# Optimization experiments

Hardware: AMD Instinct MI355X
Metric: run time of the kernel (lower is better)

Reference implementation:

```python
import jax, jax.numpy as jnp
import numpy as np

HEAD_SIZE = 64
N_EMBD = 768

def setup_inputs() -> dict:
    key = jax.random.key(0)
    k1, k2, k3, k4 = jax.random.split(key, 4)
    x = jax.random.normal(k1, (8, 2048, N_EMBD), dtype=jnp.float32)
    # nn.Linear weights are [out, in]; we store transposed [in, out] for x @ W
    scale = 1.0 / np.sqrt(N_EMBD)
    Wk = jax.random.uniform(k2, (N_EMBD, HEAD_SIZE), jnp.float32, -scale, scale)
    Wq = jax.random.uniform(k3, (N_EMBD, HEAD_SIZE), jnp.float32, -scale, scale)
    Wv = jax.random.uniform(k4, (N_EMBD, HEAD_SIZE), jnp.float32, -scale, scale)
    return {"x": x, "Wk": Wk, "Wq": Wq, "Wv": Wv}

def reference(x, Wk, Wq, Wv):
    # x: [B, T, C]
    k = x @ Wk  # [B, T, H]
    q = x @ Wq  # [B, T, H]
    v = x @ Wv  # [B, T, H]
    inv_sqrt_h = jnp.asarray(k.shape[-1], x.dtype) ** -0.5
    att = jnp.einsum('bth,bsh->bts', q, k) * inv_sqrt_h  # [B, T, T]
    att = jax.nn.softmax(att, axis=-1)  # no causal mask in original
    out = jnp.einsum('bts,bsh->bth', att, v)  # [B, T, H]
    return out
```

## Files before the change

### kernel.cpp

```cpp
#include <hip/hip_runtime.h>
#include <hip/hip_bf16.h>


#define SEQ   2048
#define CEMB  768
#define SCL 0.18033688011112042f
#define THR 11.0f

typedef __attribute__((ext_vector_type(4))) float f32x4;
typedef __attribute__((ext_vector_type(4))) float fvec4;
typedef __attribute__((ext_vector_type(8))) short short8;
typedef __attribute__((ext_vector_type(4))) short short4v;
typedef __attribute__((ext_vector_type(4))) unsigned short u16x4;
typedef __attribute__((ext_vector_type(2))) unsigned int u32x2;
typedef __attribute__((ext_vector_type(4))) unsigned int u32x4;

#define MFMA32 __builtin_amdgcn_mfma_f32_16x16x32_bf16

__device__ __forceinline__ unsigned short f2bf(float f) {
    unsigned int u = __builtin_bit_cast(unsigned int, f);
    u += 0x7fffu + ((u >> 16) & 1u);
    return (unsigned short)(u >> 16);
}
__device__ __forceinline__ unsigned int pack_bf2(float lo, float hi) {
    unsigned int ulo = __builtin_bit_cast(unsigned int, lo);
    unsigned int uhi = __builtin_bit_cast(unsigned int, hi);
    return ((uhi + 0x8000u) & 0xffff0000u) | ((ulo + 0x8000u) >> 16);
}
__device__ __forceinline__ short8 pack8(fvec4 a, fvec4 b) {
    short8 s;
    #pragma unroll
    for (int j = 0; j < 4; ++j) {
        s[j]     = (short)f2bf(a[j]);
        s[4 + j] = (short)f2bf(b[j]);
    }
    return s;
}
__device__ __forceinline__ f32x4 vmax4(f32x4 a, f32x4 b) {
    f32x4 r;
    r[0] = fmaxf(a[0], b[0]); r[1] = fmaxf(a[1], b[1]);
    r[2] = fmaxf(a[2], b[2]); r[3] = fmaxf(a[3], b[3]);
    return r;
}
__device__ __forceinline__ void gl_lds16(const void* g, void* l) {
    __builtin_amdgcn_global_load_lds(
        (const __attribute__((address_space(1))) unsigned int*)g,
        (__attribute__((address_space(3))) unsigned int*)l, 16, 0, 0);
}

__global__ void wt_kernel(const float* __restrict__ Wq, const float* __restrict__ Wk,
                          const float* __restrict__ Wv, unsigned short* __restrict__ wt) {
    int idx = blockIdx.x * 256 + threadIdx.x;
    int o = idx / 49152;
    int r = idx % 49152;
    int n = r / 768;
    int k = r % 768;
    const float* W = (o == 0) ? Wq : (o == 1) ? Wk : Wv;
    wt[idx] = f2bf(W[k * 64 + n]);
}

__global__ __launch_bounds__(768) void proj_kernel(
        const float* __restrict__ x, const unsigned short* __restrict__ wt,
        unsigned short* __restrict__ qg, unsigned short* __restrict__ kg,
        unsigned short* __restrict__ vtg) {
    __shared__ __align__(16) unsigned short xl[2][12288];

    const int tid = threadIdx.x;
    const int lane = tid & 63;
    const int wv = tid >> 6;
    const int l15 = lane & 15;
    const int lq = lane >> 4;
    const int o = wv >> 2;
    const int f = wv & 3;
    const int rowbase = blockIdx.x * 64;

    short8 wfr[24];
    #pragma unroll
    for (int s = 0; s < 24; ++s)
        wfr[s] = *reinterpret_cast<const short8*>(
            &wt[o * 49152 + (f * 16 + l15) * CEMB + s * 32 + lq * 8]);

    const int S0 = tid, S1 = 768 + tid;
    const int r0 = S0 / 96, c0 = S0 - r0 * 96;
    const int r1 = S1 / 96, c1 = S1 - r1 * 96;
    const int d0 = r0 * 1536 + ((c0 ^ (r0 & 7)) << 4);
    const int d1 = r1 * 1536 + ((c1 ^ (r1 & 7)) << 4);

    {
        const float* g0 = x + (size_t)(rowbase + r0) * CEMB + c0 * 8;
        const float* g1 = x + (size_t)(rowbase + r1) * CEMB + c1 * 8;
        fvec4 a0 = *reinterpret_cast<const fvec4*>(g0);
        fvec4 a1 = *reinterpret_cast<const fvec4*>(g0 + 4);
        fvec4 b0 = *reinterpret_cast<const fvec4*>(g1);
        fvec4 b1 = *reinterpret_cast<const fvec4*>(g1 + 4);
        *reinterpret_cast<short8*>((char*)&xl[0][0] + d0) = pack8(a0, a1);
        *reinterpret_cast<short8*>((char*)&xl[0][0] + d1) = pack8(b0, b1);
    }
    __syncthreads();

    #pragma unroll
    for (int t = 0; t < 4; ++t) {
        const int cur = t & 1;
        fvec4 pA0, pA1, pB0, pB1;
        if (t < 3) {
            const int base = rowbase + (t + 1) * 16;
            const float* g0 = x + (size_t)(base + r0) * CEMB + c0 * 8;
            const float* g1 = x + (size_t)(base + r1) * CEMB + c1 * 8;
            pA0 = *reinterpret_cast<const fvec4*>(g0);
            pA1 = *reinterpret_cast<const fvec4*>(g0 + 4);
            pB0 = *reinterpret_cast<const fvec4*>(g1);
            pB1 = *reinterpret_cast<const fvec4*>(g1 + 4);
        }

        f32x4 acc = f32x4{0.f, 0.f, 0.f, 0.f};
        const char* xb = (const char*)&xl[cur][0];
        const int rswz = l15 & 7;
        #pragma unroll
        for (int s = 0; s < 24; ++s) {
            short8 bf = *reinterpret_cast<const short8*>(
                xb + l15 * 1536 + (((s * 4 + lq) ^ rswz) << 4));
            acc = MFMA32(wfr[s], bf, acc, 0, 0, 0);
        }

        const int xrow = rowbase + t * 16 + l15;
        if (o < 2) {
            const float sc = o ? 1.f : SCL;
            u16x4 st;
            #pragma unroll
            for (int r = 0; r < 4; ++r) st[r] = f2bf(acc[r] * sc);
            unsigned short* dst = (o ? kg : qg) + (size_t)xrow * 64 + f * 16 + lq * 4;
            *reinterpret_cast<u16x4*>(dst) = st;
        } else {
            const int bb = xrow >> 11;
            const int tt = xrow & 2047;
            #pragma unroll
            for (int r = 0; r < 4; ++r)
                vtg[(size_t)bb * 131072 + (size_t)(f * 16 + lq * 4 + r) * SEQ + tt] =
                    f2bf(acc[r]);
        }

        if (t < 3) {
            *reinterpret_cast<short8*>((char*)&xl[cur ^ 1][0] + d0) = pack8(pA0, pA1);
            *reinterpret_cast<short8*>((char*)&xl[cur ^ 1][0] + d1) = pack8(pB0, pB1);
        }
        __syncthreads();
    }
}

#if __has_builtin(__builtin_amdgcn_mfma_f32_16x16x16bf16_1k)
#define HAVE_MFMA16 1
#define MFMA16 __builtin_amdgcn_mfma_f32_16x16x16bf16_1k
#else
#define HAVE_MFMA16 0
#endif

__global__ __launch_bounds__(256) void attn_kernel(
        const unsigned short* __restrict__ qg, const unsigned short* __restrict__ kg,
        const unsigned short* __restrict__ vtg, float* __restrict__ out,
        float* __restrict__ pm, float* __restrict__ pl) {
    __shared__ __align__(16) unsigned short kbuf[2][4096];
    __shared__ __align__(16) unsigned short vbuf[2][4096];

    const int tid = threadIdx.x;
    const int lane = tid & 63;
    const int wv = tid >> 6;
    const int l15 = lane & 15;
    const int lq = lane >> 4;

    const int swz = (blockIdx.x & 7) * 64 + (blockIdx.x >> 3);
    const int b = swz >> 6;
    const int qt = (swz >> 1) & 31;
    const int ks = swz & 1;
    const int qrow0 = b * SEQ + qt * 64 + wv * 16;

    const unsigned short* kgb = kg + (size_t)(b * SEQ + ks * 1024) * 64;
    const unsigned short* vgb = vtg + (size_t)b * 131072 + ks * 1024;

    const int sr0 = tid >> 3;
    const int sw0 = (((tid & 7) ^ (sr0 & 7)) * 8);
    const int sr1 = 32 + sr0;
    const int sw1 = (((tid & 7) ^ (sr1 & 7)) * 8);
    #define STAGE(S, KT) do {                                                        \
        gl_lds16(kgb + (size_t)((KT) * 64 + sr0) * 64 + sw0, &kbuf[S][tid * 8]);       \
        gl_lds16(kgb + (size_t)((KT) * 64 + sr1) * 64 + sw1, &kbuf[S][2048 + tid * 8]); \
        gl_lds16(vgb + (size_t)sr0 * SEQ + (KT) * 64 + sw0, &vbuf[S][tid * 8]);        \
        gl_lds16(vgb + (size_t)sr1 * SEQ + (KT) * 64 + sw1, &vbuf[S][2048 + tid * 8]);  \
    } while (0)

    const short8 bq0 = *reinterpret_cast<const short8*>(&qg[(size_t)(qrow0 + l15) * 64 + lq * 8]);
    const short8 bq1 = *reinterpret_cast<const short8*>(&qg[(size_t)(qrow0 + l15) * 64 + 32 + lq * 8]);

    f32x4 acc[4];
    #pragma unroll
    for (int hb = 0; hb < 4; ++hb) acc[hb] = f32x4{0.f, 0.f, 0.f, 0.f};
    float m = -3e38f, l = 0.f;

    STAGE(0, 0);
    __syncthreads();

    #define ITERL(S) do {                                                            \
        const char* kb_ = (const char*)&kbuf[S][0];                                  \
        const char* vb_ = (const char*)&vbuf[S][0];                                  \
        short8 kf[8];                                                                \
        _Pragma("unroll")                                                            \
        for (int kb = 0; kb < 4; ++kb) {                                             \
            const int row = kb * 16 + l15, rs = row & 7, rb = row * 128;             \
            kf[2 * kb]     = *reinterpret_cast<const short8*>(kb_ + rb + ((lq ^ rs) << 4));       \
            kf[2 * kb + 1] = *reinterpret_cast<const short8*>(kb_ + rb + (((lq + 4) ^ rs) << 4)); \
        }                                                                            \
        PVLOAD_L;                                                                    \
        f32x4 st[4];                                                                 \
        _Pragma("unroll")                                                            \
        for (int kb = 0; kb < 4; ++kb) {                                             \
            f32x4 z = {0.f, 0.f, 0.f, 0.f};                                          \
            st[kb] = MFMA32(kf[2 * kb], bq0, z, 0, 0, 0);                            \
            st[kb] = MFMA32(kf[2 * kb + 1], bq1, st[kb], 0, 0, 0);                   \
        }                                                                            \
        f32x4 mx = vmax4(vmax4(st[0], st[1]), vmax4(st[2], st[3]));                  \
        float p = fmaxf(fmaxf(mx[0], mx[1]), fmaxf(mx[2], mx[3]));                   \
        p = fmaxf(p, __shfl_xor(p, 16)); p = fmaxf(p, __shfl_xor(p, 32));            \
        if (__any(p > m + THR)) {                                                    \
            float mn = fmaxf(m, p);                                                  \
            float al = exp2f(m - mn);                                                \
            m = mn; l *= al;                                                         \
            _Pragma("unroll")                                                        \
            for (int hb = 0; hb < 4; ++hb)                                           \
                _Pragma("unroll")                                                    \
                for (int r = 0; r < 4; ++r) acc[hb][r] *= al;                        \
        }                                                                            \
        unsigned int w[4][2];                                                        \
        _Pragma("unroll")                                                            \
        for (int kb = 0; kb < 4; ++kb) {                                             \
            float e0 = exp2f(st[kb][0] - m), e1 = exp2f(st[kb][1] - m);              \
            float e2 = exp2f(st[kb][2] - m), e3 = exp2f(st[kb][3] - m);              \
            l += (e0 + e1) + (e2 + e3);                                              \
            w[kb][0] = pack_bf2(e0, e1); w[kb][1] = pack_bf2(e2, e3);                \
        }                                                                            \
        PVACC_L;                                                                     \
    } while (0)

#if HAVE_MFMA16
    #define PVLOAD_L                                                                 \
        short4v va[16];                                                              \
        _Pragma("unroll")                                                            \
        for (int hb = 0; hb < 4; ++hb) {                                             \
            const int row = hb * 16 + l15, rs = row & 7, rb = row * 128;             \
            _Pragma("unroll")                                                        \
            for (int kb = 0; kb < 4; ++kb)                                           \
                va[hb * 4 + kb] = *reinterpret_cast<const short4v*>(                 \
                    vb_ + rb + (((kb * 2 + (lq >> 1)) ^ rs) << 4) + (lq & 1) * 8);   \
        }
    #define PVACC_L do {                                                             \
        _Pragma("unroll")                                                            \
        for (int hb = 0; hb < 4; ++hb) {                                             \
            f32x4 a = acc[hb];                                                       \
            _Pragma("unroll")                                                        \
            for (int kb = 0; kb < 4; ++kb) {                                         \
                u32x2 uv; uv[0] = w[kb][0]; uv[1] = w[kb][1];                        \
                a = MFMA16(va[hb * 4 + kb], __builtin_bit_cast(short4v, uv), a, 0, 0, 0); \
            }                                                                        \
            acc[hb] = a;                                                             \
        }                                                                            \
    } while (0)
#else
    #define PVLOAD_L                                                                 \
        short8 va[8];                                                                \
        _Pragma("unroll")                                                            \
        for (int hb = 0; hb < 4; ++hb) {                                             \
            const int row = hb * 16 + l15, rs = row & 7, rb = row * 128;             \
            _Pragma("unroll")                                                        \
            for (int h = 0; h < 2; ++h)                                              \
                va[hb * 2 + h] = *reinterpret_cast<const short8*>(                   \
                    vb_ + rb + (((h * 4 + lq) ^ rs) << 4));                          \
        }
    #define PVACC_L do {                                                             \
        _Pragma("unroll")                                                            \
        for (int h = 0; h < 2; ++h) {                                                \
            u32x4 bw;                                                                \
            _Pragma("unroll")                                                        \
            for (int mw = 0; mw < 4; ++mw) {                                         \
                int src = l15 + ((((lq & 1) * 2) + (mw >> 1)) << 4);                 \
                unsigned int r1 = (unsigned int)__shfl((int)w[h * 2][mw & 1], src);  \
                unsigned int r2 = (unsigned int)__shfl((int)w[h * 2 + 1][mw & 1], src); \
                bw[mw] = (lq >> 1) ? r2 : r1;                                        \
            }                                                                        \
            short8 bp = __builtin_bit_cast(short8, bw);                              \
            _Pragma("unroll")                                                        \
            for (int hb = 0; hb < 4; ++hb)                                           \
                acc[hb] = MFMA32(va[hb * 2 + h], bp, acc[hb], 0, 0, 0);              \
        }                                                                            \
    } while (0)
#endif

    #pragma unroll
    for (int kt2 = 0; kt2 < 8; ++kt2) {
        const int t0 = kt2 * 2;
        if (t0 + 1 < 16) STAGE(1, t0 + 1);
        ITERL(0);
        __syncthreads();
        if (t0 + 2 < 16) STAGE(0, t0 + 2);
        ITERL(1);
        __syncthreads();
    }

    l += __shfl_xor(l, 16); l += __shfl_xor(l, 32);

    const int q = qrow0 + l15;
    char* ob = (char*)out;
    #pragma unroll
    for (int hb = 0; hb < 4; ++hb)
        #pragma unroll
        for (int r = 0; r < 4; ++r) {
            const int col = hb * 16 + lq * 4 + r;
            *reinterpret_cast<unsigned short*>(ob + ((size_t)q * 64 + col) * 4 + ks * 2) =
                f2bf(acc[hb][r]);
        }
    pm[ks * 16384 + q] = m;
    pl[ks * 16384 + q] = l;
    #undef STAGE
    #undef ITERL
    #undef PVLOAD_L
    #undef PVACC_L
}

__global__ __launch_bounds__(256) void combine_kernel(
        float* __restrict__ out, const float* __restrict__ pm,
        const float* __restrict__ pl) {
    const int idx = blockIdx.x * 256 + threadIdx.x;
    const int w0 = idx * 4;
    const int q = w0 >> 6;
    u32x4 d = *reinterpret_cast<const u32x4*>(reinterpret_cast<const unsigned int*>(out) + w0);
    const float m0 = pm[q], m1 = pm[16384 + q];
    const float l0 = pl[q], l1 = pl[16384 + q];
    const float M = fmaxf(m0, m1);
    const float e0 = exp2f(m0 - M), e1 = exp2f(m1 - M);
    const float inv = 1.0f / (l0 * e0 + l1 * e1);
    fvec4 r;
    #pragma unroll
    for (int j = 0; j < 4; ++j) {
        float p0 = __builtin_bit_cast(float, d[j] << 16);
        float p1 = __builtin_bit_cast(float, d[j] & 0xffff0000u);
        r[j] = (p0 * e0 + p1 * e1) * inv;
    }
    *reinterpret_cast<fvec4*>(out + w0) = r;
}

extern "C" void kernel_launch(void* const* d_in, const int* in_sizes, int n_in,
                              void* d_out, int out_size, void* d_ws, size_t ws_size,
                              hipStream_t stream) {
    (void)in_sizes; (void)n_in; (void)out_size; (void)ws_size;
    const float* x  = (const float*)d_in[0];
    const float* Wk = (const float*)d_in[1];
    const float* Wq = (const float*)d_in[2];
    const float* Wv = (const float*)d_in[3];
    float* out = (float*)d_out;

    unsigned short* ws = (unsigned short*)d_ws;
    unsigned short* qg  = ws;
    unsigned short* kg  = ws + 1048576;
    unsigned short* vtg = ws + 2097152;
    unsigned short* wt  = ws + 3145728;
    float* pm = (float*)((char*)d_ws + 6586368);
    float* pl = pm + 32768;

    wt_kernel<<<576, 256, 0, stream>>>(Wq, Wk, Wv, wt);
    proj_kernel<<<256, 768, 0, stream>>>(x, wt, qg, kg, vtg);
    attn_kernel<<<512, 256, 0, stream>>>(qg, kg, vtg, out, pm, pl);
    combine_kernel<<<1024, 256, 0, stream>>>(out, pm, pl);
}
```

Before: 60.47 us.

## Process two query subtiles per wave and split keys four ways in attention

The attention kernel now has each wave handle 32 query rows (two 16-row subtiles) against each staged K/V tile, so every LDS fragment load is reused twice. Keys are split into four 512-long chunks instead of two, keeping the grid at 512 blocks. Partial outputs go to a separate bf16 buffer, and a rewritten combine kernel merges four partials. The projection kernel prefetches x two tiles ahead and writes the next LDS buffer before the epilogue. This adds register pressure (two accumulator sets), more partial-output traffic and a heavier combine step.

New measurement: 55.11 us, median of 3. -8.9%, faster.

```diff
diff --git a/kernel.cpp b/kernel.cpp
--- a/kernel.cpp
+++ b/kernel.cpp
@@ -12,8 +12,8 @@
 typedef __attribute__((ext_vector_type(8))) short short8;
 typedef __attribute__((ext_vector_type(4))) short short4v;
 typedef __attribute__((ext_vector_type(4))) unsigned short u16x4;
+typedef __attribute__((ext_vector_type(8))) unsigned short u16x8;
 typedef __attribute__((ext_vector_type(2))) unsigned int u32x2;
-typedef __attribute__((ext_vector_type(4))) unsigned int u32x4;
 
 #define MFMA32 __builtin_amdgcn_mfma_f32_16x16x32_bf16
 
@@ -21,6 +21,9 @@
     unsigned int u = __builtin_bit_cast(unsigned int, f);
     u += 0x7fffu + ((u >> 16) & 1u);
     return (unsigned short)(u >> 16);
+}
+__device__ __forceinline__ float bf2f(unsigned short s) {
+    return __builtin_bit_cast(float, (unsigned int)s << 16);
 }
 __device__ __forceinline__ unsigned int pack_bf2(float lo, float hi) {
     unsigned int ulo = __builtin_bit_cast(unsigned int, lo);
@@ -86,31 +89,30 @@
     const int d0 = r0 * 1536 + ((c0 ^ (r0 & 7)) << 4);
     const int d1 = r1 * 1536 + ((c1 ^ (r1 & 7)) << 4);
 
+    #define LOADT(PA0, PA1, PB0, PB1, T) do {                               \
+        const float* g0_ = x + (size_t)(rowbase + (T) * 16 + r0) * CEMB + c0 * 8; \
+        const float* g1_ = x + (size_t)(rowbase + (T) * 16 + r1) * CEMB + c1 * 8; \
+        PA0 = *reinterpret_cast<const fvec4*>(g0_);                         \
+        PA1 = *reinterpret_cast<const fvec4*>(g0_ + 4);                     \
+        PB0 = *reinterpret_cast<const fvec4*>(g1_);                         \
+        PB1 = *reinterpret_cast<const fvec4*>(g1_ + 4);                     \
+    } while (0)
+
+    fvec4 pb[2][4];
     {
-        const float* g0 = x + (size_t)(rowbase + r0) * CEMB + c0 * 8;
-        const float* g1 = x + (size_t)(rowbase + r1) * CEMB + c1 * 8;
-        fvec4 a0 = *reinterpret_cast<const fvec4*>(g0);
-        fvec4 a1 = *reinterpret_cast<const fvec4*>(g0 + 4);
-        fvec4 b0 = *reinterpret_cast<const fvec4*>(g1);
-        fvec4 b1 = *reinterpret_cast<const fvec4*>(g1 + 4);
+        fvec4 a0, a1, b0, b1;
+        LOADT(a0, a1, b0, b1, 0);
         *reinterpret_cast<short8*>((char*)&xl[0][0] + d0) = pack8(a0, a1);
         *reinterpret_cast<short8*>((char*)&xl[0][0] + d1) = pack8(b0, b1);
+        LOADT(pb[0][0], pb[0][1], pb[0][2], pb[0][3], 1);
     }
     __syncthreads();
 
     #pragma unroll
     for (int t = 0; t < 4; ++t) {
         const int cur = t & 1;
-        fvec4 pA0, pA1, pB0, pB1;
-        if (t < 3) {
-            const int base = rowbase + (t + 1) * 16;
-            const float* g0 = x + (size_t)(base + r0) * CEMB + c0 * 8;
-            const float* g1 = x + (size_t)(base + r1) * CEMB + c1 * 8;
-            pA0 = *reinterpret_cast<const fvec4*>(g0);
-            pA1 = *reinterpret_cast<const fvec4*>(g0 + 4);
-            pB0 = *reinterpret_cast<const fvec4*>(g1);
-            pB1 = *reinterpret_cast<const fvec4*>(g1 + 4);
-        }
+        if (t < 2)
+            LOADT(pb[cur ^ 1][0], pb[cur ^ 1][1], pb[cur ^ 1][2], pb[cur ^ 1][3], t + 2);
 
         f32x4 acc = f32x4{0.f, 0.f, 0.f, 0.f};
         const char* xb = (const char*)&xl[cur][0];
@@ -120,6 +122,13 @@
             short8 bf = *reinterpret_cast<const short8*>(
                 xb + l15 * 1536 + (((s * 4 + lq) ^ rswz) << 4));
             acc = MFMA32(wfr[s], bf, acc, 0, 0, 0);
+        }
+
+        if (t < 3) {
+            *reinterpret_cast<short8*>((char*)&xl[cur ^ 1][0] + d0) =
+                pack8(pb[cur][0], pb[cur][1]);
+            *reinterpret_cast<short8*>((char*)&xl[cur ^ 1][0] + d1) =
+                pack8(pb[cur][2], pb[cur][3]);
         }
 
         const int xrow = rowbase + t * 16 + l15;
@@ -138,13 +147,9 @@
                 vtg[(size_t)bb * 131072 + (size_t)(f * 16 + lq * 4 + r) * SEQ + tt] =
                     f2bf(acc[r]);
         }
-
-        if (t < 3) {
-            *reinterpret_cast<short8*>((char*)&xl[cur ^ 1][0] + d0) = pack8(pA0, pA1);
-            *reinterpret_cast<short8*>((char*)&xl[cur ^ 1][0] + d1) = pack8(pB0, pB1);
-        }
         __syncthreads();
     }
+    #undef LOADT
 }
 
 #if __has_builtin(__builtin_amdgcn_mfma_f32_16x16x16bf16_1k)
@@ -156,7 +161,7 @@
 
 __global__ __launch_bounds__(256) void attn_kernel(
         const unsigned short* __restrict__ qg, const unsigned short* __restrict__ kg,
-        const unsigned short* __restrict__ vtg, float* __restrict__ out,
+        const unsigned short* __restrict__ vtg, unsigned short* __restrict__ pO,
         float* __restrict__ pm, float* __restrict__ pl) {
     __shared__ __align__(16) unsigned short kbuf[2][4096];
     __shared__ __align__(16) unsigned short vbuf[2][4096];
@@ -169,12 +174,12 @@
 
     const int swz = (blockIdx.x & 7) * 64 + (blockIdx.x >> 3);
     const int b = swz >> 6;
-    const int qt = (swz >> 1) & 31;
-    const int ks = swz & 1;
-    const int qrow0 = b * SEQ + qt * 64 + wv * 16;
-
-    const unsigned short* kgb = kg + (size_t)(b * SEQ + ks * 1024) * 64;
-    const unsigned short* vgb = vtg + (size_t)b * 131072 + ks * 1024;
+    const int qt = (swz >> 2) & 15;
+    const int ks = swz & 3;
+    const int qrow0 = b * SEQ + qt * 128 + wv * 32;
+
+    const unsigned short* kgb = kg + (size_t)(b * SEQ + ks * 512) * 64;
+    const unsigned short* vgb = vtg + (size_t)b * 131072 + ks * 512;
 
     const int sr0 = tid >> 3;
     const int sw0 = (((tid & 7) ^ (sr0 & 7)) * 8);
@@ -187,56 +192,51 @@
         gl_lds16(vgb + (size_t)sr1 * SEQ + (KT) * 64 + sw1, &vbuf[S][2048 + tid * 8]);  \
     } while (0)
 
-    const short8 bq0 = *reinterpret_cast<const short8*>(&qg[(size_t)(qrow0 + l15) * 64 + lq * 8]);
-    const short8 bq1 = *reinterpret_cast<const short8*>(&qg[(size_t)(qrow0 + l15) * 64 + 32 + lq * 8]);
-
-    f32x4 acc[4];
-    #pragma unroll
-    for (int hb = 0; hb < 4; ++hb) acc[hb] = f32x4{0.f, 0.f, 0.f, 0.f};
-    float m = -3e38f, l = 0.f;
+    const short8 bq00 = *reinterpret_cast<const short8*>(&qg[(size_t)(qrow0 + l15) * 64 + lq * 8]);
+    const short8 bq01 = *reinterpret_cast<const short8*>(&qg[(size_t)(qrow0 + l15) * 64 + 32 + lq * 8]);
+    const short8 bq10 = *reinterpret_cast<const short8*>(&qg[(size_t)(qrow0 + 16 + l15) * 64 + lq * 8]);
+    const short8 bq11 = *reinterpret_cast<const short8*>(&qg[(size_t)(qrow0 + 16 + l15) * 64 + 32 + lq * 8]);
+
+    f32x4 acc0[4], acc1[4];
+    #pragma unroll
+    for (int hb = 0; hb < 4; ++hb) {
+        acc0[hb] = f32x4{0.f, 0.f, 0.f, 0.f};
+        acc1[hb] = f32x4{0.f, 0.f, 0.f, 0.f};
+    }
+    float m0 = -3e38f, m1 = -3e38f, l0 = 0.f, l1 = 0.f;
 
     STAGE(0, 0);
     __syncthreads();
 
-    #define ITERL(S) do {                                                            \
-        const char* kb_ = (const char*)&kbuf[S][0];                                  \
-        const char* vb_ = (const char*)&vbuf[S][0];                                  \
-        short8 kf[8];                                                                \
-        _Pragma("unroll")                                                            \
-        for (int kb = 0; kb < 4; ++kb) {                                             \
-            const int row = kb * 16 + l15, rs = row & 7, rb = row * 128;             \
-            kf[2 * kb]     = *reinterpret_cast<const short8*>(kb_ + rb + ((lq ^ rs) << 4));       \
-            kf[2 * kb + 1] = *reinterpret_cast<const short8*>(kb_ + rb + (((lq + 4) ^ rs) << 4)); \
-        }                                                                            \
-        PVLOAD_L;                                                                    \
+    #define SUBITER(BQ0, BQ1, MM, LL, ACC) do {                                      \
         f32x4 st[4];                                                                 \
         _Pragma("unroll")                                                            \
         for (int kb = 0; kb < 4; ++kb) {                                             \
             f32x4 z = {0.f, 0.f, 0.f, 0.f};                                          \
-            st[kb] = MFMA32(kf[2 * kb], bq0, z, 0, 0, 0);                            \
-            st[kb] = MFMA32(kf[2 * kb + 1], bq1, st[kb], 0, 0, 0);                   \
+            st[kb] = MFMA32(kf[2 * kb], BQ0, z, 0, 0, 0);                            \
+            st[kb] = MFMA32(kf[2 * kb + 1], BQ1, st[kb], 0, 0, 0);                   \
         }                                                                            \
         f32x4 mx = vmax4(vmax4(st[0], st[1]), vmax4(st[2], st[3]));                  \
         float p = fmaxf(fmaxf(mx[0], mx[1]), fmaxf(mx[2], mx[3]));                   \
         p = fmaxf(p, __shfl_xor(p, 16)); p = fmaxf(p, __shfl_xor(p, 32));            \
-        if (__any(p > m + THR)) {                                                    \
-            float mn = fmaxf(m, p);                                                  \
-            float al = exp2f(m - mn);                                                \
-            m = mn; l *= al;                                                         \
+        if (__any(p > MM + THR)) {                                                   \
+            float mn = fmaxf(MM, p);                                                 \
+            float al = exp2f(MM - mn);                                               \
+            MM = mn; LL *= al;                                                       \
             _Pragma("unroll")                                                        \
             for (int hb = 0; hb < 4; ++hb)                                           \
                 _Pragma("unroll")                                                    \
-                for (int r = 0; r < 4; ++r) acc[hb][r] *= al;                        \
+                for (int r = 0; r < 4; ++r) ACC[hb][r] *= al;                        \
         }                                                                            \
         unsigned int w[4][2];                                                        \
         _Pragma("unroll")                                                            \
         for (int kb = 0; kb < 4; ++kb) {                                             \
-            float e0 = exp2f(st[kb][0] - m), e1 = exp2f(st[kb][1] - m);              \
-            float e2 = exp2f(st[kb][2] - m), e3 = exp2f(st[kb][3] - m);              \
-            l += (e0 + e1) + (e2 + e3);                                              \
+            float e0 = exp2f(st[kb][0] - MM), e1 = exp2f(st[kb][1] - MM);            \
+            float e2 = exp2f(st[kb][2] - MM), e3 = exp2f(st[kb][3] - MM);            \
+            LL += (e0 + e1) + (e2 + e3);                                             \
             w[kb][0] = pack_bf2(e0, e1); w[kb][1] = pack_bf2(e2, e3);                \
         }                                                                            \
-        PVACC_L;                                                                     \
+        PVACC_L(w, ACC);                                                             \
     } while (0)
 
 #if HAVE_MFMA16
@@ -250,16 +250,16 @@
                 va[hb * 4 + kb] = *reinterpret_cast<const short4v*>(                 \
                     vb_ + rb + (((kb * 2 + (lq >> 1)) ^ rs) << 4) + (lq & 1) * 8);   \
         }
-    #define PVACC_L do {                                                             \
+    #define PVACC_L(W, ACC) do {                                                     \
         _Pragma("unroll")                                                            \
         for (int hb = 0; hb < 4; ++hb) {                                             \
-            f32x4 a = acc[hb];                                                       \
+            f32x4 a = ACC[hb];                                                       \
             _Pragma("unroll")                                                        \
             for (int kb = 0; kb < 4; ++kb) {                                         \
-                u32x2 uv; uv[0] = w[kb][0]; uv[1] = w[kb][1];                        \
+                u32x2 uv; uv[0] = W[kb][0]; uv[1] = W[kb][1];                        \
                 a = MFMA16(va[hb * 4 + kb], __builtin_bit_cast(short4v, uv), a, 0, 0, 0); \
             }                                                                        \
-            acc[hb] = a;                                                             \
+            ACC[hb] = a;                                                             \
         }                                                                            \
     } while (0)
 #else
@@ -273,76 +273,130 @@
                 va[hb * 2 + h] = *reinterpret_cast<const short8*>(                   \
                     vb_ + rb + (((h * 4 + lq) ^ rs) << 4));                          \
         }
-    #define PVACC_L do {                                                             \
+    #define PVACC_L(W, ACC) do {                                                     \
         _Pragma("unroll")                                                            \
         for (int h = 0; h < 2; ++h) {                                                \
-            u32x4 bw;                                                                \
-            _Pragma("unroll")                                                        \
-            for (int mw = 0; mw < 4; ++mw) {                                         \
-                int src = l15 + ((((lq & 1) * 2) + (mw >> 1)) << 4);                 \
-                unsigned int r1 = (unsigned int)__shfl((int)w[h * 2][mw & 1], src);  \
-                unsigned int r2 = (unsigned int)__shfl((int)w[h * 2 + 1][mw & 1], src); \
-                bw[mw] = (lq >> 1) ? r2 : r1;                                        \
+            unsigned int bw0, bw1, bw2, bw3;                                         \
+            {                                                                        \
+                int src0 = l15 + (((lq & 1) * 2) << 4);                              \
+                int src1 = l15 + ((((lq & 1) * 2) + 1) << 4);                        \
+                unsigned int a0 = (unsigned int)__shfl((int)W[h * 2][0], src0);      \
+                unsigned int a1 = (unsigned int)__shfl((int)W[h * 2 + 1][0], src0);  \
+                unsigned int b0 = (unsigned int)__shfl((int)W[h * 2][1], src0);      \
+                unsigned int b1 = (unsigned int)__shfl((int)W[h * 2 + 1][1], src0);  \
+                unsigned int c0_ = (unsigned int)__shfl((int)W[h * 2][0], src1);     \
+                unsigned int c1_ = (unsigned int)__shfl((int)W[h * 2 + 1][0], src1); \
+                unsigned int d0_ = (unsigned int)__shfl((int)W[h * 2][1], src1);     \
+                unsigned int d1_ = (unsigned int)__shfl((int)W[h * 2 + 1][1], src1); \
+                bw0 = (lq >> 1) ? a1 : a0; bw1 = (lq >> 1) ? b1 : b0;                \
+                bw2 = (lq >> 1) ? c1_ : c0_; bw3 = (lq >> 1) ? d1_ : d0_;            \
             }                                                                        \
-            short8 bp = __builtin_bit_cast(short8, bw);                              \
+            short8 bp;                                                               \
+            {                                                                        \
+                unsigned int t_[4] = {bw0, bw2, bw1, bw3};                           \
+                bp = *reinterpret_cast<short8*>(t_);                                 \
+            }                                                                        \
             _Pragma("unroll")                                                        \
             for (int hb = 0; hb < 4; ++hb)                                           \
-                acc[hb] = MFMA32(va[hb * 2 + h], bp, acc[hb], 0, 0, 0);              \
+                ACC[hb] = MFMA32(va[hb * 2 + h], bp, ACC[hb], 0, 0, 0);              \
         }                                                                            \
     } while (0)
 #endif
 
-    #pragma unroll
-    for (int kt2 = 0; kt2 < 8; ++kt2) {
+    #define ITERL(S) do {                                                            \
+        const char* kb_ = (const char*)&kbuf[S][0];                                  \
+        const char* vb_ = (const char*)&vbuf[S][0];                                  \
+        short8 kf[8];                                                                \
+        _Pragma("unroll")                                                            \
+        for (int kb = 0; kb < 4; ++kb) {                                             \
+            const int row = kb * 16 + l15, rs = row & 7, rb = row * 128;             \
+            kf[2 * kb]     = *reinterpret_cast<const short8*>(kb_ + rb + ((lq ^ rs) << 4));       \
+            kf[2 * kb + 1] = *reinterpret_cast<const short8*>(kb_ + rb + (((lq + 4) ^ rs) << 4)); \
+        }                                                                            \
+        PVLOAD_L;                                                                    \
+        SUBITER(bq00, bq01, m0, l0, acc0);                                           \
+        SUBITER(bq10, bq11, m1, l1, acc1);                                           \
+    } while (0)
+
+    #pragma unroll
+    for (int kt2 = 0; kt2 < 4; ++kt2) {
         const int t0 = kt2 * 2;
-        if (t0 + 1 < 16) STAGE(1, t0 + 1);
+        if (t0 + 1 < 8) STAGE(1, t0 + 1);
         ITERL(0);
         __syncthreads();
-        if (t0 + 2 < 16) STAGE(0, t0 + 2);
+        if (t0 + 2 < 8) STAGE(0, t0 + 2);
         ITERL(1);
         __syncthreads();
     }
 
-    l += __shfl_xor(l, 16); l += __shfl_xor(l, 32);
-
-    const int q = qrow0 + l15;
-    char* ob = (char*)out;
-    #pragma unroll
-    for (int hb = 0; hb < 4; ++hb)
+    l0 += __shfl_xor(l0, 16); l0 += __shfl_xor(l0, 32);
+    l1 += __shfl_xor(l1, 16); l1 += __shfl_xor(l1, 32);
+
+    #pragma unroll
+    for (int s = 0; s < 2; ++s) {
+        const int q = qrow0 + s * 16 + l15;
+        f32x4* ac = s ? acc1 : acc0;
         #pragma unroll
-        for (int r = 0; r < 4; ++r) {
-            const int col = hb * 16 + lq * 4 + r;
-            *reinterpret_cast<unsigned short*>(ob + ((size_t)q * 64 + col) * 4 + ks * 2) =
-                f2bf(acc[hb][r]);
-        }
-    pm[ks * 16384 + q] = m;
-    pl[ks * 16384 + q] = l;
+        for (int hb = 0; hb < 4; ++hb) {
+            u16x4 st;
+            #pragma unroll
+            for (int r = 0; r < 4; ++r) st[r] = f2bf(ac[hb][r]);
+            *reinterpret_cast<u16x4*>(&pO[((size_t)(ks * 16384 + q)) * 64 + hb * 16 + lq * 4]) = st;
+        }
+        pm[ks * 16384 + q] = s ? m1 : m0;
+        pl[ks * 16384 + q] = s ? l1 : l0;
+    }
     #undef STAGE
     #undef ITERL
+    #undef SUBITER
     #undef PVLOAD_L
     #undef PVACC_L
 }
 
 __global__ __launch_bounds__(256) void combine_kernel(
-        float* __restrict__ out, const float* __restrict__ pm,
-        const float* __restrict__ pl) {
+        float* __restrict__ out, const unsigned short* __restrict__ pO,
+        const float* __restrict__ pm, const float* __restrict__ pl) {
     const int idx = blockIdx.x * 256 + threadIdx.x;
-    const int w0 = idx * 4;
-    const int q = w0 >> 6;
-    u32x4 d = *reinterpret_cast<const u32x4*>(reinterpret_cast<const unsigned int*>(out) + w0);
-    const float m0 = pm[q], m1 = pm[16384 + q];
-    const float l0 = pl[q], l1 = pl[16384 + q];
-    const float M = fmaxf(m0, m1);
-    const float e0 = exp2f(m0 - M), e1 = exp2f(m1 - M);
-    const float inv = 1.0f / (l0 * e0 + l1 * e1);
-    fvec4 r;
-    #pragma unroll
-    for (int j = 0; j < 4; ++j) {
-        float p0 = __builtin_bit_cast(float, d[j] << 16);
-        float p1 = __builtin_bit_cast(float, d[j] & 0xffff0000u);
-        r[j] = (p0 * e0 + p1 * e1) * inv;
-    }
-    *reinterpret_cast<fvec4*>(out + w0) = r;
+    const int q = idx >> 2;
+    const int c0 = (idx & 3) * 16;
+
+    float mv[4], lv[4];
+    #pragma unroll
+    for (int k = 0; k < 4; ++k) {
+        mv[k] = pm[k * 16384 + q];
+        lv[k] = pl[k * 16384 + q];
+    }
+    float M = fmaxf(fmaxf(mv[0], mv[1]), fmaxf(mv[2], mv[3]));
+    float e[4], L = 0.f;
+    #pragma unroll
+    for (int k = 0; k < 4; ++k) {
+        e[k] = exp2f(mv[k] - M);
+        L += lv[k] * e[k];
+    }
+    const float inv = 1.0f / L;
+
+    float res[16];
+    #pragma unroll
+    for (int j = 0; j < 16; ++j) res[j] = 0.f;
+    #pragma unroll
+    for (int k = 0; k < 4; ++k) {
+        const unsigned short* p = &pO[((size_t)(k * 16384 + q)) * 64 + c0];
+        u16x8 a = *reinterpret_cast<const u16x8*>(p);
+        u16x8 b = *reinterpret_cast<const u16x8*>(p + 8);
+        #pragma unroll
+        for (int j = 0; j < 8; ++j) {
+            res[j]     += e[k] * bf2f(a[j]);
+            res[8 + j] += e[k] * bf2f(b[j]);
+        }
+    }
+    float* op = &out[(size_t)q * 64 + c0];
+    #pragma unroll
+    for (int v = 0; v < 4; ++v) {
+        fvec4 r;
+        #pragma unroll
+        for (int j = 0; j < 4; ++j) r[j] = res[v * 4 + j] * inv;
+        *reinterpret_cast<fvec4*>(op + v * 4) = r;
+    }
 }
 
 extern "C" void kernel_launch(void* const* d_in, const int* in_sizes, int n_in,
@@ -361,10 +415,11 @@
     unsigned short* vtg = ws + 2097152;
     unsigned short* wt  = ws + 3145728;
     float* pm = (float*)((char*)d_ws + 6586368);
-    float* pl = pm + 32768;
+    float* pl = pm + 65536;
+    unsigned short* pO = (unsigned short*)((char*)d_ws + 7110656);
 
     wt_kernel<<<576, 256, 0, stream>>>(Wq, Wk, Wv, wt);
     proj_kernel<<<256, 768, 0, stream>>>(x, wt, qg, kg, vtg);
-    attn_kernel<<<512, 256, 0, stream>>>(qg, kg, vtg, out, pm, pl);
-    combine_kernel<<<1024, 256, 0, stream>>>(out, pm, pl);
-}
+    attn_kernel<<<512, 256, 0, stream>>>(qg, kg, vtg, pO, pm, pl);
+    combine_kernel<<<256, 256, 0, stream>>>(out, pO, pm, pl);
+}
```
